# Kernel tuning notes

Hardware: AMD Instinct MI355X
Metric: run time of the kernel (lower is better)

The kernel has to match this reference:

```python
import jax, jax.numpy as jnp
import numpy as np

NUM_HEADER = 8
DIM_HIDDEN = 512
DIM_HEADER = DIM_HIDDEN // NUM_HEADER


def setup_inputs() -> dict:
    key = jax.random.key(0)
    ks = jax.random.split(key, 11)
    B, S, D = 2, 4096, DIM_HIDDEN
    scale = 1.0 / np.sqrt(D)
    inp = {
        "q": jax.random.normal(ks[0], (B, S, D), jnp.float32),
        "k": jax.random.normal(ks[1], (B, S, D), jnp.float32),
        "v": jax.random.normal(ks[2], (B, S, D), jnp.float32),
        # nn.Linear weights are [out, in]; y = x @ W.T + b
        "Wq": jax.random.normal(ks[3], (D, D), jnp.float32) * scale,
        "bq": jax.random.normal(ks[4], (D,), jnp.float32) * scale,
        "Wk": jax.random.normal(ks[5], (D, D), jnp.float32) * scale,
        "bk": jax.random.normal(ks[6], (D,), jnp.float32) * scale,
        "Wv": jax.random.normal(ks[7], (D, D), jnp.float32) * scale,
        "bv": jax.random.normal(ks[8], (D,), jnp.float32) * scale,
        "Wo": jax.random.normal(ks[9], (D, D), jnp.float32) * scale,
        "bo": jax.random.normal(ks[10], (D,), jnp.float32) * scale,
    }
    return inp


def reference(q, k, v, Wq, bq, Wk, bk, Wv, bv, Wo, bo):
    B = q.shape[0]
    H, dh = NUM_HEADER, DIM_HEADER

    def proj(x, W, b):
        # [B,S,D] -> [B,H,S,dh]
        y = jnp.einsum('bsd,ed->bse', x, W) + b
        return y.reshape(B, -1, H, dh).transpose(0, 2, 1, 3)

    qh = proj(q, Wq, bq)
    kh = proj(k, Wk, bk)
    vh = proj(v, Wv, bv)

    scores = jnp.einsum('bhqd,bhkd->bhqk', qh, kh) / jnp.sqrt(jnp.float32(dh))
    attn = jax.nn.softmax(scores, axis=-1)
    ctx = jnp.einsum('bhqk,bhkd->bhqd', attn, vh)
    concat = ctx.transpose(0, 2, 1, 3).reshape(B, -1, H * dh)
    return jnp.einsum('bsd,ed->bse', concat, Wo) + bo
```

## Files before the change

kernel.cpp:

```cpp
#include <hip/hip_runtime.h>
#include <hip/hip_bf16.h>

typedef __attribute__((ext_vector_type(8))) short short8;
typedef __attribute__((ext_vector_type(4))) float f32x4;
typedef __attribute__((ext_vector_type(16))) float f32x16;
typedef __attribute__((ext_vector_type(4))) float f4v;

#define SEQ 4096
#define NBH 16
#define SCALE_Q 0.18033688011112042f

#define MFMA16(a, b, c) __builtin_amdgcn_mfma_f32_16x16x32_bf16(a, b, c, 0, 0, 0)
#define MFMA32(a, b, c) __builtin_amdgcn_mfma_f32_32x32x16_bf16(a, b, c, 0, 0, 0)

__device__ __forceinline__ short f2bf(float f) {
  union { float f; unsigned u; } x; x.f = f;
  unsigned r = x.u + 0x7FFFu + ((x.u >> 16) & 1u);
  return (short)(r >> 16);
}

__device__ __forceinline__ unsigned cvt_pk_bf16(float lo, float hi) {
  unsigned r;
  asm("v_cvt_pk_bf16_f32 %0, %1, %2" : "=v"(r) : "v"(lo), "v"(hi));
  return r;
}

__device__ __forceinline__ short8 cvt8(const float* __restrict__ src) {
  f4v v0 = *(const f4v*)src;
  f4v v1 = *(const f4v*)(src + 4);
  union { unsigned u[4]; short8 s; } r;
  r.u[0] = cvt_pk_bf16(v0[0], v0[1]);
  r.u[1] = cvt_pk_bf16(v0[2], v0[3]);
  r.u[2] = cvt_pk_bf16(v1[0], v1[1]);
  r.u[3] = cvt_pk_bf16(v1[2], v1[3]);
  return r.s;
}

__device__ __forceinline__ void gll16(const void* g, void* l) {
  __builtin_amdgcn_global_load_lds(
      (const __attribute__((address_space(1))) void*)g,
      (__attribute__((address_space(3))) void*)l, 16, 0, 0);
}

__device__ __forceinline__ void pswap(unsigned& a, unsigned& b) {
  asm volatile("v_permlane32_swap_b32 %0, %1" : "+v"(a), "+v"(b));
}

__global__ __launch_bounds__(256) void cvt_w(
    const float* __restrict__ w0, const float* __restrict__ w1,
    const float* __restrict__ w2, const float* __restrict__ w3,
    short* __restrict__ dst)
{
  int i = blockIdx.x * 256 + threadIdx.x;
  int m = i >> 15;
  int off = (i & 32767) * 8;
  const float* s = (m == 0) ? w0 : (m == 1) ? w1 : (m == 2) ? w2 : w3;
  *(short8*)(dst + (size_t)m * 262144 + off) = cvt8(s + off);
}

template <int MODE>
__global__ __launch_bounds__(256) void gemm_bt(
    const float* __restrict__ Af, const short* __restrict__ Ab,
    const short* __restrict__ Wb, const float* __restrict__ bias,
    void* __restrict__ Cout)
{
  __shared__ __align__(16) char smemA[64 * 72 * 2];
  __shared__ __align__(16) char smemB[128 * 64 * 2];
  short (*As)[72] = (short(*)[72])smemA;
  const int t    = threadIdx.x;
  const int lane = t & 63;
  const int w    = t >> 6;
  const int g    = lane >> 4;
  const int q    = lane & 15;
  const int tile_n = blockIdx.x * 128;
  const int tile_m = blockIdx.y * 64;

  f32x4 acc[4][2];
#pragma unroll
  for (int mi = 0; mi < 4; ++mi)
#pragma unroll
    for (int ni = 0; ni < 2; ++ni)
#pragma unroll
      for (int j = 0; j < 4; ++j) acc[mi][ni][j] = 0.f;

  for (int k0 = 0; k0 < 512; k0 += 64) {
    __syncthreads();
    if (MODE != 3) {
#pragma unroll
      for (int it = 0; it < 2; ++it) {
        int i = it * 256 + t;
        int r = i >> 3, sg = i & 7;
        *(short8*)&As[r][sg * 8] =
            cvt8(Af + (size_t)(tile_m + r) * 512 + k0 + sg * 8);
      }
    } else {
#pragma unroll
      for (int it = 0; it < 2; ++it) {
        int i = it * 256 + t;
        int row = i >> 3, cg = i & 7;
        const char* gp = (const char*)Ab +
            ((size_t)(tile_m + row) * 512 + k0) * 2 + ((cg ^ (row & 7)) << 4);
        gll16(gp, smemA + (size_t)(it * 256 + (t & ~63)) * 16);
      }
    }
#pragma unroll
    for (int it = 0; it < 4; ++it) {
      int i = it * 256 + t;
      int row = i >> 3, cg = i & 7;
      const char* gp = (const char*)Wb +
          ((size_t)(tile_n + row) * 512 + k0) * 2 + ((cg ^ (row & 7)) << 4);
      gll16(gp, smemB + (size_t)(it * 256 + (t & ~63)) * 16);
    }
    __syncthreads();
#pragma unroll
    for (int kk = 0; kk < 2; ++kk) {
      short8 af[4], bfv[2];
#pragma unroll
      for (int mi = 0; mi < 4; ++mi) {
        int rA = mi * 16 + q;
        if (MODE != 3)
          af[mi] = *(const short8*)&As[rA][kk * 32 + g * 8];
        else
          af[mi] = *(const short8*)(smemA + rA * 128 +
                                    (((4 * kk + g) ^ (rA & 7)) << 4));
      }
#pragma unroll
      for (int ni = 0; ni < 2; ++ni) {
        int rB = w * 32 + ni * 16 + q;
        bfv[ni] = *(const short8*)(smemB + rB * 128 +
                                   (((4 * kk + g) ^ (rB & 7)) << 4));
      }
#pragma unroll
      for (int mi = 0; mi < 4; ++mi)
#pragma unroll
        for (int ni = 0; ni < 2; ++ni) {
          if (MODE == 2)
            acc[mi][ni] = MFMA16(bfv[ni], af[mi], acc[mi][ni]);
          else
            acc[mi][ni] = MFMA16(af[mi], bfv[ni], acc[mi][ni]);
        }
    }
  }

#pragma unroll
  for (int mi = 0; mi < 4; ++mi) {
#pragma unroll
    for (int ni = 0; ni < 2; ++ni) {
#pragma unroll
      for (int j = 0; j < 4; ++j) {
        if (MODE == 2) {
          int e = tile_n + w * 32 + ni * 16 + 4 * g + j;
          int srow = tile_m + mi * 16 + q;
          float val = acc[mi][ni][j] + bias[e];
          int b = srow >> 12, sl = srow & 4095;
          int h = e >> 6, d = e & 63;
          ((short*)Cout)[((size_t)((b * 8 + h) * 64 + d)) * SEQ + sl] = f2bf(val);
        } else {
          int m = tile_m + mi * 16 + g * 4 + j;
          int e = tile_n + w * 32 + ni * 16 + q;
          float val = acc[mi][ni][j] + bias[e];
          if (MODE == 0) val *= SCALE_Q;
          if (MODE == 3) {
            ((float*)Cout)[(size_t)m * 512 + e] = val;
          } else {
            int b = m >> 12, s = m & 4095;
            int h = e >> 6, d = e & 63;
            ((short*)Cout)[((size_t)(b * 8 + h) * SEQ + s) * 64 + d] = f2bf(val);
          }
        }
      }
    }
  }
}

__global__ __launch_bounds__(256) void attn_kernel(
    const short* __restrict__ Qh, const short* __restrict__ Kh,
    const short* __restrict__ Vt, short* __restrict__ ctx)
{
  __shared__ __align__(16) char smem[2][16384];
  const int t    = threadIdx.x;
  const int lane = t & 63;
  const int w    = t >> 6;
  const int l31  = lane & 31;
  const int hi   = lane >> 5;

  const int fid = blockIdx.x;
  const int lid = (fid & 7) * 64 + (fid >> 3);
  const int qt  = lid & 31;
  const int bh  = lid >> 5;

  const size_t kbase = (size_t)bh * SEQ * 64;
  const size_t vbase = (size_t)bh * 64 * SEQ;
  const int q0 = qt * 128 + w * 32;

  short8 qf[4];
#pragma unroll
  for (int m = 0; m < 4; ++m)
    qf[m] = *(const short8*)(Qh + kbase + (size_t)(q0 + l31) * 64 + m * 16 + hi * 8);

  f32x16 fz;
#pragma unroll
  for (int r = 0; r < 16; ++r) fz[r] = 0.f;
  f32x16 acc0 = fz, acc1 = fz;
  float mrun = -1e30f, lrun = 0.f;

  const int rif  = lane >> 3;
  const int scol = ((lane & 7) ^ rif) * 16;
  const int xr   = (hi * 16) ^ ((lane & 7) << 4);

#define STAGE(buf, kt)                                                         \
  {                                                                            \
    _Pragma("unroll")                                                          \
    for (int i = 0; i < 4; ++i) {                                              \
      int c = w * 4 + i;                                                       \
      char* ldst = &smem[buf][c * 1024];                                       \
      if (c < 8) {                                                             \
        int row = c * 8 + rif;                                                 \
        const char* gp = (const char*)Kh +                                     \
            ((kbase + (size_t)((kt) * 64 + row) * 64) * 2 + scol);             \
        gll16(gp, ldst);                                                       \
      } else {                                                                 \
        int row = (c - 8) * 8 + rif;                                           \
        const char* gp = (const char*)Vt +                                     \
            ((vbase + (size_t)row * SEQ + (kt) * 64) * 2 + scol);              \
        gll16(gp, ldst);                                                       \
      }                                                                        \
    }                                                                          \
  }

  STAGE(0, 0);
  int cur = 0;

  for (int kt = 0; kt < SEQ / 64; ++kt) {
    if (kt < SEQ / 64 - 1) {
      STAGE(cur ^ 1, kt + 1);
      asm volatile("s_waitcnt vmcnt(4)" ::: "memory");
    } else {
      asm volatile("s_waitcnt vmcnt(0)" ::: "memory");
    }
    __builtin_amdgcn_sched_barrier(0);
    __builtin_amdgcn_s_barrier();
    __builtin_amdgcn_sched_barrier(0);

    const char* Kb = &smem[cur][0];
    const char* Vb = &smem[cur][8192];

    f32x16 s0, s1;
    {
      short8 k0 = *(const short8*)(Kb + (size_t)(l31) * 128 + ((32 * 0) ^ xr));
      short8 k1 = *(const short8*)(Kb + (size_t)(32 + l31) * 128 + ((32 * 0) ^ xr));
      __builtin_amdgcn_s_setprio(1);
      s0 = MFMA32(k0, qf[0], fz);
      s1 = MFMA32(k1, qf[0], fz);
      __builtin_amdgcn_s_setprio(0);
    }
#pragma unroll
    for (int m = 1; m < 4; ++m) {
      short8 k0 = *(const short8*)(Kb + (size_t)(l31) * 128 + ((32 * m) ^ xr));
      short8 k1 = *(const short8*)(Kb + (size_t)(32 + l31) * 128 + ((32 * m) ^ xr));
      __builtin_amdgcn_s_setprio(1);
      s0 = MFMA32(k0, qf[m], s0);
      s1 = MFMA32(k1, qf[m], s1);
      __builtin_amdgcn_s_setprio(0);
    }

    float a_[16];
#pragma unroll
    for (int r = 0; r < 16; ++r) a_[r] = fmaxf(s0[r], s1[r]);
#pragma unroll
    for (int r = 0; r < 8; ++r) a_[r] = fmaxf(a_[r], a_[r + 8]);
#pragma unroll
    for (int r = 0; r < 4; ++r) a_[r] = fmaxf(a_[r], a_[r + 4]);
    float pm = fmaxf(fmaxf(a_[0], a_[1]), fmaxf(a_[2], a_[3]));
    pm = fmaxf(pm, __shfl_xor(pm, 32));

    const bool skip = __all(pm <= mrun + 11.0f);
    const float mnew = skip ? mrun : fmaxf(mrun, pm);

#pragma unroll
    for (int r = 0; r < 16; ++r) {
      s0[r] = __builtin_amdgcn_exp2f(s0[r] - mnew);
      s1[r] = __builtin_amdgcn_exp2f(s1[r] - mnew);
    }

    float b_[16];
#pragma unroll
    for (int r = 0; r < 16; ++r) b_[r] = s0[r] + s1[r];
#pragma unroll
    for (int r = 0; r < 8; ++r) b_[r] += b_[r + 8];
#pragma unroll
    for (int r = 0; r < 4; ++r) b_[r] += b_[r + 4];
    float rs = (b_[0] + b_[1]) + (b_[2] + b_[3]);
    rs += __shfl_xor(rs, 32);

    if (!skip) {
      float corr = __builtin_amdgcn_exp2f(mrun - mnew);
      lrun = lrun * corr + rs;
      mrun = mnew;
#pragma unroll
      for (int r = 0; r < 16; ++r) {
        float cr = __shfl(corr, ((r & 3) + 8 * (r >> 2)) + 4 * hi);
        acc0[r] *= cr;
        acc1[r] *= cr;
      }
    } else {
      lrun += rs;
    }

    union { unsigned u[4]; short8 v; } A0[2], A1[2];
#pragma unroll
    for (int c = 0; c < 2; ++c) {
      const f32x16& s = c ? s1 : s0;
      unsigned pk0 = cvt_pk_bf16(s[0], s[1]);
      unsigned pk1 = cvt_pk_bf16(s[2], s[3]);
      unsigned pk2 = cvt_pk_bf16(s[4], s[5]);
      unsigned pk3 = cvt_pk_bf16(s[6], s[7]);
      unsigned pk4 = cvt_pk_bf16(s[8], s[9]);
      unsigned pk5 = cvt_pk_bf16(s[10], s[11]);
      unsigned pk6 = cvt_pk_bf16(s[12], s[13]);
      unsigned pk7 = cvt_pk_bf16(s[14], s[15]);
      pswap(pk0, pk2);
      pswap(pk1, pk3);
      pswap(pk4, pk6);
      pswap(pk5, pk7);
      A0[c].u[0] = pk0; A0[c].u[1] = pk1; A0[c].u[2] = pk2; A0[c].u[3] = pk3;
      A1[c].u[0] = pk4; A1[c].u[1] = pk5; A1[c].u[2] = pk6; A1[c].u[3] = pk7;
    }

#pragma unroll
    for (int c = 0; c < 2; ++c) {
#pragma unroll
      for (int h2 = 0; h2 < 2; ++h2) {
        short8 pa = h2 ? A1[c].v : A0[c].v;
        short8 vf0 = *(const short8*)(Vb + (size_t)(l31) * 128 +
                                      ((64 * c + 32 * h2) ^ xr));
        short8 vf1 = *(const short8*)(Vb + (size_t)(32 + l31) * 128 +
                                      ((64 * c + 32 * h2) ^ xr));
        __builtin_amdgcn_s_setprio(1);
        acc0 = MFMA32(pa, vf0, acc0);
        acc1 = MFMA32(pa, vf1, acc1);
        __builtin_amdgcn_s_setprio(0);
      }
    }

    __builtin_amdgcn_sched_barrier(0);
    __builtin_amdgcn_s_barrier();
    __builtin_amdgcn_sched_barrier(0);
    cur ^= 1;
  }

  const int b = bh >> 3, hh = bh & 7;
  const float inv = 1.0f / lrun;
#pragma unroll
  for (int r = 0; r < 16; ++r) {
    int ql = (r & 3) + 8 * (r >> 2) + 4 * hi;
    float iv = __shfl(inv, ql);
    int qrow = q0 + ql;
    size_t off = ((size_t)(b * SEQ + qrow)) * 512 + hh * 64 + l31;
    ctx[off]      = f2bf(acc0[r] * iv);
    ctx[off + 32] = f2bf(acc1[r] * iv);
  }
}

extern "C" void kernel_launch(void* const* d_in, const int* in_sizes, int n_in,
                              void* d_out, int out_size, void* d_ws, size_t ws_size,
                              hipStream_t stream) {
  const float* q  = (const float*)d_in[0];
  const float* k  = (const float*)d_in[1];
  const float* v  = (const float*)d_in[2];
  const float* Wq = (const float*)d_in[3];
  const float* bq = (const float*)d_in[4];
  const float* Wk = (const float*)d_in[5];
  const float* bk = (const float*)d_in[6];
  const float* Wv = (const float*)d_in[7];
  const float* bv = (const float*)d_in[8];
  const float* Wo = (const float*)d_in[9];
  const float* bo = (const float*)d_in[10];

  const size_t NELT = (size_t)NBH * SEQ * 64;
  short* Qh  = (short*)d_ws;
  short* Kh  = Qh + NELT;
  short* Vt  = Kh + NELT;
  short* ctx = Vt + NELT;
  short* Wb  = ctx + NELT;

  dim3 tb(256);
  cvt_w<<<dim3(512), tb, 0, stream>>>(Wq, Wk, Wv, Wo, Wb);

  dim3 gb(4, 128);
  gemm_bt<0><<<gb, tb, 0, stream>>>(q, nullptr, Wb,          bq, (void*)Qh);
  gemm_bt<1><<<gb, tb, 0, stream>>>(k, nullptr, Wb + 262144, bk, (void*)Kh);
  gemm_bt<2><<<gb, tb, 0, stream>>>(v, nullptr, Wb + 524288, bv, (void*)Vt);
  attn_kernel<<<dim3(512), tb, 0, stream>>>(Qh, Kh, Vt, ctx);
  gemm_bt<3><<<gb, tb, 0, stream>>>(nullptr, ctx, Wb + 786432, bo, d_out);
}
```

Baseline: 171.7 us.

## Split attention over KV halves with a merge kernel and interleaved softmax

Adds a two-way split of the key/value sequence so 1024 attention blocks run instead of 512, writing fp32 partial outputs plus running max and sum that a new merge kernel combines into bf16 context. The softmax is reordered so the exp, row sum and bf16 pack for each 32-key half feed their PV MFMAs directly, which shortens live ranges. Launch bounds now request 4 blocks per SM. The aim is to fill more of the GPU's compute units and overlap exp with MFMA. The cost is extra fp32 partial traffic, an additional kernel launch, and a fallback path when workspace is too small.

Result: no change. 172.2 us (+0.3%).

```diff
diff --git a/kernel.cpp b/kernel.cpp
--- a/kernel.cpp
+++ b/kernel.cpp
@@ -173,9 +173,11 @@
   }
 }
 
-__global__ __launch_bounds__(256) void attn_kernel(
+template <int NSPLIT>
+__global__ __launch_bounds__(256, 4) void attn_kernel(
     const short* __restrict__ Qh, const short* __restrict__ Kh,
-    const short* __restrict__ Vt, short* __restrict__ ctx)
+    const short* __restrict__ Vt, short* __restrict__ ctx,
+    float* __restrict__ Opart, float* __restrict__ ml)
 {
   __shared__ __align__(16) char smem[2][16384];
   const int t    = threadIdx.x;
@@ -185,9 +187,16 @@
   const int hi   = lane >> 5;
 
   const int fid = blockIdx.x;
-  const int lid = (fid & 7) * 64 + (fid >> 3);
-  const int qt  = lid & 31;
-  const int bh  = lid >> 5;
+  int qt, bh, split;
+  if (NSPLIT == 1) {
+    int lid = (fid & 7) * 64 + (fid >> 3);
+    qt = lid & 31; bh = lid >> 5; split = 0;
+  } else {
+    int lid = (fid & 7) * 128 + (fid >> 3);
+    qt = lid & 31; split = (lid >> 5) & 1; bh = lid >> 6;
+  }
+  const int NT  = (SEQ / 64) / NSPLIT;
+  const int kt0 = split * NT;
 
   const size_t kbase = (size_t)bh * SEQ * 64;
   const size_t vbase = (size_t)bh * 64 * SEQ;
@@ -228,11 +237,12 @@
     }                                                                          \
   }
 
-  STAGE(0, 0);
+  STAGE(0, kt0);
   int cur = 0;
 
-  for (int kt = 0; kt < SEQ / 64; ++kt) {
-    if (kt < SEQ / 64 - 1) {
+  for (int it = 0; it < NT; ++it) {
+    const int kt = kt0 + it;
+    if (it < NT - 1) {
       STAGE(cur ^ 1, kt + 1);
       asm volatile("s_waitcnt vmcnt(4)" ::: "memory");
     } else {
@@ -277,25 +287,9 @@
     const bool skip = __all(pm <= mrun + 11.0f);
     const float mnew = skip ? mrun : fmaxf(mrun, pm);
 
-#pragma unroll
-    for (int r = 0; r < 16; ++r) {
-      s0[r] = __builtin_amdgcn_exp2f(s0[r] - mnew);
-      s1[r] = __builtin_amdgcn_exp2f(s1[r] - mnew);
-    }
-
-    float b_[16];
-#pragma unroll
-    for (int r = 0; r < 16; ++r) b_[r] = s0[r] + s1[r];
-#pragma unroll
-    for (int r = 0; r < 8; ++r) b_[r] += b_[r + 8];
-#pragma unroll
-    for (int r = 0; r < 4; ++r) b_[r] += b_[r + 4];
-    float rs = (b_[0] + b_[1]) + (b_[2] + b_[3]);
-    rs += __shfl_xor(rs, 32);
-
     if (!skip) {
       float corr = __builtin_amdgcn_exp2f(mrun - mnew);
-      lrun = lrun * corr + rs;
+      lrun *= corr;
       mrun = mnew;
 #pragma unroll
       for (int r = 0; r < 16; ++r) {
@@ -303,45 +297,82 @@
         acc0[r] *= cr;
         acc1[r] *= cr;
       }
-    } else {
-      lrun += rs;
-    }
-
-    union { unsigned u[4]; short8 v; } A0[2], A1[2];
-#pragma unroll
-    for (int c = 0; c < 2; ++c) {
-      const f32x16& s = c ? s1 : s0;
-      unsigned pk0 = cvt_pk_bf16(s[0], s[1]);
-      unsigned pk1 = cvt_pk_bf16(s[2], s[3]);
-      unsigned pk2 = cvt_pk_bf16(s[4], s[5]);
-      unsigned pk3 = cvt_pk_bf16(s[6], s[7]);
-      unsigned pk4 = cvt_pk_bf16(s[8], s[9]);
-      unsigned pk5 = cvt_pk_bf16(s[10], s[11]);
-      unsigned pk6 = cvt_pk_bf16(s[12], s[13]);
-      unsigned pk7 = cvt_pk_bf16(s[14], s[15]);
-      pswap(pk0, pk2);
-      pswap(pk1, pk3);
-      pswap(pk4, pk6);
-      pswap(pk5, pk7);
-      A0[c].u[0] = pk0; A0[c].u[1] = pk1; A0[c].u[2] = pk2; A0[c].u[3] = pk3;
-      A1[c].u[0] = pk4; A1[c].u[1] = pk5; A1[c].u[2] = pk6; A1[c].u[3] = pk7;
-    }
-
-#pragma unroll
-    for (int c = 0; c < 2; ++c) {
-#pragma unroll
-      for (int h2 = 0; h2 < 2; ++h2) {
-        short8 pa = h2 ? A1[c].v : A0[c].v;
-        short8 vf0 = *(const short8*)(Vb + (size_t)(l31) * 128 +
-                                      ((64 * c + 32 * h2) ^ xr));
-        short8 vf1 = *(const short8*)(Vb + (size_t)(32 + l31) * 128 +
-                                      ((64 * c + 32 * h2) ^ xr));
-        __builtin_amdgcn_s_setprio(1);
-        acc0 = MFMA32(pa, vf0, acc0);
-        acc1 = MFMA32(pa, vf1, acc1);
-        __builtin_amdgcn_s_setprio(0);
-      }
-    }
+    }
+
+#pragma unroll
+    for (int r = 0; r < 16; ++r) s0[r] = __builtin_amdgcn_exp2f(s0[r] - mnew);
+    float rs0;
+    {
+      float b_[8];
+#pragma unroll
+      for (int r = 0; r < 8; ++r) b_[r] = s0[r] + s0[r + 8];
+#pragma unroll
+      for (int r = 0; r < 4; ++r) b_[r] += b_[r + 4];
+      rs0 = (b_[0] + b_[1]) + (b_[2] + b_[3]);
+    }
+    union { unsigned u[4]; short8 v; } A0c, A1c;
+    {
+      unsigned p0 = cvt_pk_bf16(s0[0], s0[1]);
+      unsigned p1 = cvt_pk_bf16(s0[2], s0[3]);
+      unsigned p2 = cvt_pk_bf16(s0[4], s0[5]);
+      unsigned p3 = cvt_pk_bf16(s0[6], s0[7]);
+      unsigned p4 = cvt_pk_bf16(s0[8], s0[9]);
+      unsigned p5 = cvt_pk_bf16(s0[10], s0[11]);
+      unsigned p6 = cvt_pk_bf16(s0[12], s0[13]);
+      unsigned p7 = cvt_pk_bf16(s0[14], s0[15]);
+      pswap(p0, p2); pswap(p1, p3); pswap(p4, p6); pswap(p5, p7);
+      A0c.u[0] = p0; A0c.u[1] = p1; A0c.u[2] = p2; A0c.u[3] = p3;
+      A1c.u[0] = p4; A1c.u[1] = p5; A1c.u[2] = p6; A1c.u[3] = p7;
+    }
+#pragma unroll
+    for (int h2 = 0; h2 < 2; ++h2) {
+      short8 pa = h2 ? A1c.v : A0c.v;
+      short8 vf0 = *(const short8*)(Vb + (size_t)(l31) * 128 + ((32 * h2) ^ xr));
+      short8 vf1 = *(const short8*)(Vb + (size_t)(32 + l31) * 128 + ((32 * h2) ^ xr));
+      __builtin_amdgcn_s_setprio(1);
+      acc0 = MFMA32(pa, vf0, acc0);
+      acc1 = MFMA32(pa, vf1, acc1);
+      __builtin_amdgcn_s_setprio(0);
+    }
+
+#pragma unroll
+    for (int r = 0; r < 16; ++r) s1[r] = __builtin_amdgcn_exp2f(s1[r] - mnew);
+    float rs1;
+    {
+      float b_[8];
+#pragma unroll
+      for (int r = 0; r < 8; ++r) b_[r] = s1[r] + s1[r + 8];
+#pragma unroll
+      for (int r = 0; r < 4; ++r) b_[r] += b_[r + 4];
+      rs1 = (b_[0] + b_[1]) + (b_[2] + b_[3]);
+    }
+    {
+      unsigned p0 = cvt_pk_bf16(s1[0], s1[1]);
+      unsigned p1 = cvt_pk_bf16(s1[2], s1[3]);
+      unsigned p2 = cvt_pk_bf16(s1[4], s1[5]);
+      unsigned p3 = cvt_pk_bf16(s1[6], s1[7]);
+      unsigned p4 = cvt_pk_bf16(s1[8], s1[9]);
+      unsigned p5 = cvt_pk_bf16(s1[10], s1[11]);
+      unsigned p6 = cvt_pk_bf16(s1[12], s1[13]);
+      unsigned p7 = cvt_pk_bf16(s1[14], s1[15]);
+      pswap(p0, p2); pswap(p1, p3); pswap(p4, p6); pswap(p5, p7);
+      A0c.u[0] = p0; A0c.u[1] = p1; A0c.u[2] = p2; A0c.u[3] = p3;
+      A1c.u[0] = p4; A1c.u[1] = p5; A1c.u[2] = p6; A1c.u[3] = p7;
+    }
+#pragma unroll
+    for (int h2 = 0; h2 < 2; ++h2) {
+      short8 pa = h2 ? A1c.v : A0c.v;
+      short8 vf0 = *(const short8*)(Vb + (size_t)(l31) * 128 + ((64 + 32 * h2) ^ xr));
+      short8 vf1 = *(const short8*)(Vb + (size_t)(32 + l31) * 128 + ((64 + 32 * h2) ^ xr));
+      __builtin_amdgcn_s_setprio(1);
+      acc0 = MFMA32(pa, vf0, acc0);
+      acc1 = MFMA32(pa, vf1, acc1);
+      __builtin_amdgcn_s_setprio(0);
+    }
+
+    float rs = rs0 + rs1;
+    rs += __shfl_xor(rs, 32);
+    lrun += rs;
 
     __builtin_amdgcn_sched_barrier(0);
     __builtin_amdgcn_s_barrier();
@@ -349,17 +380,66 @@
     cur ^= 1;
   }
 
-  const int b = bh >> 3, hh = bh & 7;
-  const float inv = 1.0f / lrun;
-#pragma unroll
-  for (int r = 0; r < 16; ++r) {
-    int ql = (r & 3) + 8 * (r >> 2) + 4 * hi;
-    float iv = __shfl(inv, ql);
-    int qrow = q0 + ql;
-    size_t off = ((size_t)(b * SEQ + qrow)) * 512 + hh * 64 + l31;
-    ctx[off]      = f2bf(acc0[r] * iv);
-    ctx[off + 32] = f2bf(acc1[r] * iv);
-  }
+  if (NSPLIT == 1) {
+    const int b = bh >> 3, hh = bh & 7;
+    const float inv = 1.0f / lrun;
+#pragma unroll
+    for (int r = 0; r < 16; ++r) {
+      int ql = (r & 3) + 8 * (r >> 2) + 4 * hi;
+      float iv = __shfl(inv, ql);
+      int qrow = q0 + ql;
+      size_t off = ((size_t)(b * SEQ + qrow)) * 512 + hh * 64 + l31;
+      ctx[off]      = f2bf(acc0[r] * iv);
+      ctx[off + 32] = f2bf(acc1[r] * iv);
+    }
+  } else {
+    float* Ob = Opart + (((size_t)(split * NBH + bh) * SEQ + q0)) * 64;
+#pragma unroll
+    for (int r = 0; r < 16; ++r) {
+      int ql = (r & 3) + 8 * (r >> 2) + 4 * hi;
+      Ob[(size_t)ql * 64 + l31]      = acc0[r];
+      Ob[(size_t)ql * 64 + l31 + 32] = acc1[r];
+    }
+    if (hi == 0) {
+      size_t mi_ = ((size_t)(split * NBH + bh) * SEQ + q0 + l31) * 2;
+      ml[mi_]     = mrun;
+      ml[mi_ + 1] = lrun;
+    }
+  }
+}
+
+__global__ __launch_bounds__(256) void merge_kernel(
+    const float* __restrict__ Opart, const float* __restrict__ ml,
+    short* __restrict__ ctx)
+{
+  int idx = blockIdx.x * 256 + threadIdx.x;
+  int dg = idx & 7;
+  int qq = (idx >> 3) & 4095;
+  int bh = idx >> 15;
+  size_t r0 = (size_t)bh * SEQ + qq;
+  size_t r1 = (size_t)(NBH + bh) * SEQ + qq;
+  float m0 = ml[r0 * 2], l0 = ml[r0 * 2 + 1];
+  float m1 = ml[r1 * 2], l1 = ml[r1 * 2 + 1];
+  float mm = fmaxf(m0, m1);
+  float c0 = __builtin_amdgcn_exp2f(m0 - mm);
+  float c1 = __builtin_amdgcn_exp2f(m1 - mm);
+  float inv = 1.0f / (l0 * c0 + l1 * c1);
+  c0 *= inv; c1 *= inv;
+  const float* o0 = Opart + r0 * 64 + dg * 8;
+  const float* o1 = Opart + r1 * 64 + dg * 8;
+  f4v a0 = *(const f4v*)o0, a1 = *(const f4v*)(o0 + 4);
+  f4v b0 = *(const f4v*)o1, b1 = *(const f4v*)(o1 + 4);
+  float v[8];
+#pragma unroll
+  for (int j = 0; j < 4; ++j) v[j] = a0[j] * c0 + b0[j] * c1;
+#pragma unroll
+  for (int j = 0; j < 4; ++j) v[4 + j] = a1[j] * c0 + b1[j] * c1;
+  union { unsigned u[4]; short8 s; } r;
+  r.u[0] = cvt_pk_bf16(v[0], v[1]);
+  r.u[1] = cvt_pk_bf16(v[2], v[3]);
+  r.u[2] = cvt_pk_bf16(v[4], v[5]);
+  r.u[3] = cvt_pk_bf16(v[6], v[7]);
+  *(short8*)(ctx + ((size_t)(bh >> 3) * SEQ + qq) * 512 + (bh & 7) * 64 + dg * 8) = r.s;
 }
 
 extern "C" void kernel_launch(void* const* d_in, const int* in_sizes, int n_in,
@@ -383,6 +463,11 @@
   short* Vt  = Kh + NELT;
   short* ctx = Vt + NELT;
   short* Wb  = ctx + NELT;
+  float* Opart = (float*)(Wb + 4 * 262144);
+  float* ml    = Opart + 2 * (size_t)NBH * SEQ * 64;
+  const size_t needed = (size_t)(ml + 2 * (size_t)NBH * SEQ * 2 - (float*)0) -
+                        (size_t)((float*)d_ws - (float*)0);
+  const bool split2 = ws_size >= needed * 4;
 
   dim3 tb(256);
   cvt_w<<<dim3(512), tb, 0, stream>>>(Wq, Wk, Wv, Wo, Wb);
@@ -391,6 +476,11 @@
   gemm_bt<0><<<gb, tb, 0, stream>>>(q, nullptr, Wb,          bq, (void*)Qh);
   gemm_bt<1><<<gb, tb, 0, stream>>>(k, nullptr, Wb + 262144, bk, (void*)Kh);
   gemm_bt<2><<<gb, tb, 0, stream>>>(v, nullptr, Wb + 524288, bv, (void*)Vt);
-  attn_kernel<<<dim3(512), tb, 0, stream>>>(Qh, Kh, Vt, ctx);
+  if (split2) {
+    attn_kernel<2><<<dim3(1024), tb, 0, stream>>>(Qh, Kh, Vt, ctx, Opart, ml);
+    merge_kernel<<<dim3(NBH * SEQ * 8 / 256), tb, 0, stream>>>(Opart, ml, ctx);
+  } else {
+    attn_kernel<1><<<dim3(512), tb, 0, stream>>>(Qh, Kh, Vt, ctx, Opart, ml);
+  }
   gemm_bt<3><<<gb, tb, 0, stream>>>(nullptr, ctx, Wb + 786432, bo, d_out);
 }
```
